# Optimization experiments

Measured on AMD Instinct MI355X. Metric: run time of the kernel, lower is better.

The kernel has to match this reference:

```python
import jax, jax.numpy as jnp
import numpy as np

EPS = 1e-7

def _attend(x):
    # x: [nc, w, h]; faithful to SelfAttention_1 with patch_size=3 (1x1 kernels, padding=1)
    nc, w, h = x.shape
    L = w * h
    # per-location 1x1 kernels, L2-normalized (kernels are [L, nc, 1, 1] in torch)
    k = x.reshape(nc, L).T + EPS                      # [L, nc]
    k = k / jnp.sqrt(jnp.sum(k * k, axis=1, keepdims=True))
    # conv2d with 1x1 kernels and padding=1 -> scores on padded grid [L, w+2, h+2]
    xp = jnp.pad(x, ((0, 0), (1, 1), (1, 1)))
    s = jnp.einsum('lc,cuv->luv', k, xp)              # [L, w+2, h+2]
    # avg_pool2d(3,1,pad=1) * 9 == 3x3 sum pooling with zero padding
    s = jax.lax.reduce_window(s, 0.0, jax.lax.add, (1, 3, 3), (1, 1, 1),
                              ((0, 0), (1, 1), (1, 1)))
    a = jax.nn.softmax(s, axis=0)                     # softmax over L (channel) axis
    # conv_transpose2d with 1x1 kernels, padding=1 == crop border then K^T @ A
    out = jnp.einsum('lc,luv->cuv', k, a[:, 1:-1, 1:-1])  # [nc, w, h]
    # torch: attention_scores.permute(0,2,3,1).view(w*h, -1) (raw reshape)
    att = jnp.transpose(a, (1, 2, 0)).reshape(L, -1)  # [L, (w+2)*(h+2)]
    return out, att


def setup_inputs() -> dict:
    key = jax.random.key(0)
    foreground = jax.random.normal(key, (4, 256, 64, 64), dtype=jnp.float32)
    return {"foreground": foreground}


def reference(foreground):
    out, att = jax.vmap(_attend)(foreground)          # out: [bz,nc,w,h], att: [bz,L,(w+2)*(h+2)]
    bz, L, M = att.shape
    return out, att.reshape(bz * L, M)
```

## Files before the change

kernel.cpp:

```cpp
#include <hip/hip_runtime.h>
#include <math.h>
#include <stdint.h>

#define LDIM 4096
#define NC   256
#define W66  66
#define P66  4356
#define BZ   4
#define EPSK 1e-7f

typedef _Float16 v8h __attribute__((ext_vector_type(8)));
typedef float v4f __attribute__((ext_vector_type(4)));

__device__ __forceinline__ void cp16(const void* g, void* l) {
    __builtin_amdgcn_global_load_lds(
        (const __attribute__((address_space(1))) void*)g,
        (__attribute__((address_space(3))) void*)l, 16, 0, 0);
}

__global__ __launch_bounds__(256) void rnorm_kernel(const float* __restrict__ x,
                                                    float* __restrict__ rnorm) {
    int idx = blockIdx.x * 256 + threadIdx.x;
    int b = idx >> 12;
    int l = idx & (LDIM - 1);
    const float* xb = x + (size_t)b * NC * LDIM + l;
    float s = 0.f;
#pragma unroll 8
    for (int c = 0; c < NC; ++c) {
        float v = xb[(size_t)c * LDIM] + EPSK;
        s += v * v;
    }
    rnorm[idx] = 1.0f / sqrtf(s);
}

__global__ __launch_bounds__(256) void kconv_kernel(const float* __restrict__ x,
                                                    const float* __restrict__ rn,
                                                    _Float16* __restrict__ Kcl,
                                                    _Float16* __restrict__ Klc) {
    __shared__ _Float16 t[64][72];
    int b = blockIdx.z, c0 = blockIdx.y * 64, l0 = blockIdx.x * 64;
    int tid = threadIdx.x;
    int r = tid >> 2, q = (tid & 3) * 16;
    const float* xr = x + ((size_t)(b * NC + c0 + r)) * LDIM + l0 + q;
    const float* rr = rn + b * LDIM + l0 + q;
    _Float16 h[16];
#pragma unroll
    for (int j = 0; j < 16; ++j)
        h[j] = (_Float16)((xr[j] + EPSK) * rr[j]);
    _Float16* kc = Kcl + ((size_t)(b * NC + c0 + r)) * LDIM + l0 + q;
    *(v8h*)kc = *(v8h*)h;
    *(v8h*)(kc + 8) = *(v8h*)(h + 8);
#pragma unroll
    for (int j = 0; j < 16; ++j) t[r][q + j] = h[j];
    __syncthreads();
    _Float16 g[16];
#pragma unroll
    for (int j = 0; j < 16; ++j) g[j] = t[q + j][r];
    _Float16* kl = Klc + ((size_t)(b * LDIM + l0 + r)) * NC + c0 + q;
    *(v8h*)kl = *(v8h*)g;
    *(v8h*)(kl + 8) = *(v8h*)(g + 8);
}

__global__ __launch_bounds__(256) void pool_kernel(const float* __restrict__ x,
                                                   float* __restrict__ Pm) {
    size_t idx = (size_t)blockIdx.x * 256 + threadIdx.x;
    int p = (int)(idx % P66);
    size_t bc = idx / P66;
    int u = p / W66, v = p % W66;
    const float* xbc = x + bc * (size_t)LDIM;
    int i0 = max(u - 2, 0), i1 = min(u, 63);
    int j0 = max(v - 2, 0), j1 = min(v, 63);
    float s = 0.f;
    for (int i = i0; i <= i1; ++i)
        for (int j = j0; j <= j1; ++j)
            s += xbc[i * 64 + j];
    Pm[idx] = s;
}

__global__ __launch_bounds__(256) void ptrans_kernel(const float* __restrict__ PoolF,
                                                     _Float16* __restrict__ Pm16) {
    __shared__ float t[64][65];
    int b = blockIdx.z, c0 = blockIdx.y * 64, p0 = blockIdx.x * 64;
    int tid = threadIdx.x;
    int r = tid >> 2, q = (tid & 3) * 16;
    const float* src = PoolF + ((size_t)(b * NC + c0 + r)) * P66 + p0 + q;
#pragma unroll
    for (int j = 0; j < 16; ++j) t[r][q + j] = src[j];
    __syncthreads();
    if (p0 + r < P66) {
        _Float16 g[16];
#pragma unroll
        for (int j = 0; j < 16; ++j) g[j] = (_Float16)t[q + j][r];
        _Float16* dst = Pm16 + ((size_t)(b * P66 + p0 + r)) * NC + c0 + q;
        *(v8h*)dst = *(v8h*)g;
        *(v8h*)(dst + 8) = *(v8h*)(g + 8);
    }
}

__global__ __launch_bounds__(256) void gemm1_mfma(const _Float16* __restrict__ Pm16,
                                                  const _Float16* __restrict__ Klc,
                                                  float* __restrict__ S) {
    __shared__ _Float16 As[128 * 32];
    __shared__ _Float16 Bs[128 * 32];
    int b = blockIdx.z;
    int p0 = blockIdx.y * 128;
    int l0 = blockIdx.x * 128;
    const _Float16* A = Pm16 + (size_t)b * P66 * NC;
    const _Float16* B = Klc + (size_t)b * LDIM * NC;
    float* C = S + (size_t)b * P66 * LDIM;
    int tid = threadIdx.x;
    int lane = tid & 63, wave = tid >> 6;
    int wm = (wave >> 1) * 64, wn = (wave & 1) * 64;
    int quad = lane >> 4, hn = lane & 15;
    int sr = tid >> 2, sk = (tid & 3) * 8;
    int pa0 = p0 + sr;      if (pa0 > P66 - 1) pa0 = P66 - 1;
    int pa1 = p0 + sr + 64; if (pa1 > P66 - 1) pa1 = P66 - 1;
    const _Float16* Ag0 = A + (size_t)pa0 * NC + sk;
    const _Float16* Ag1 = A + (size_t)pa1 * NC + sk;
    const _Float16* Bg0 = B + (size_t)(l0 + sr) * NC + sk;
    const _Float16* Bg1 = B + (size_t)(l0 + sr + 64) * NC + sk;
    char* lA = (char*)As + tid * 16;
    char* lB = (char*)Bs + tid * 16;
    v4f acc[4][4];
    v4f vz = {0.f, 0.f, 0.f, 0.f};
#pragma unroll
    for (int i = 0; i < 4; ++i)
#pragma unroll
        for (int j = 0; j < 4; ++j) acc[i][j] = vz;

    for (int k0 = 0; k0 < NC; k0 += 32) {
        __syncthreads();
        cp16(Ag0 + k0, lA);
        cp16(Ag1 + k0, lA + 4096);
        cp16(Bg0 + k0, lB);
        cp16(Bg1 + k0, lB + 4096);
        __syncthreads();
        v8h af[4], bfr[4];
#pragma unroll
        for (int t = 0; t < 4; ++t)
            af[t] = *(const v8h*)(As + (wm + t * 16 + hn) * 32 + quad * 8);
#pragma unroll
        for (int t = 0; t < 4; ++t)
            bfr[t] = *(const v8h*)(Bs + (wn + t * 16 + hn) * 32 + quad * 8);
#pragma unroll
        for (int i = 0; i < 4; ++i)
#pragma unroll
            for (int j = 0; j < 4; ++j)
                acc[i][j] = __builtin_amdgcn_mfma_f32_16x16x32_f16(af[i], bfr[j], acc[i][j], 0, 0, 0);
    }
#pragma unroll
    for (int i = 0; i < 4; ++i) {
        int pr = p0 + wm + i * 16 + quad * 4;
#pragma unroll
        for (int j = 0; j < 4; ++j) {
            int lc = l0 + wn + j * 16 + hn;
            float* Cp = C + (size_t)pr * LDIM + lc;
#pragma unroll
            for (int r = 0; r < 4; ++r)
                if (pr + r < P66) Cp[(size_t)r * LDIM] = acc[i][j][r];
        }
    }
}

__global__ __launch_bounds__(256) void softmax_kernel(float* __restrict__ att) {
    float* row = att + (size_t)blockIdx.x * LDIM;
    int tid = threadIdx.x;
    float4 v[4];
    float mx = -1e30f;
#pragma unroll
    for (int i = 0; i < 4; ++i) {
        v[i] = ((float4*)row)[tid + i * 256];
        mx = fmaxf(mx, fmaxf(fmaxf(v[i].x, v[i].y), fmaxf(v[i].z, v[i].w)));
    }
    __shared__ float sred[4];
    __shared__ float ssum[4];
#pragma unroll
    for (int off = 32; off > 0; off >>= 1) mx = fmaxf(mx, __shfl_xor(mx, off));
    if ((tid & 63) == 0) sred[tid >> 6] = mx;
    __syncthreads();
    float m4 = fmaxf(fmaxf(sred[0], sred[1]), fmaxf(sred[2], sred[3]));
    float sum = 0.f;
#pragma unroll
    for (int i = 0; i < 4; ++i) {
        v[i].x = __expf(v[i].x - m4);
        v[i].y = __expf(v[i].y - m4);
        v[i].z = __expf(v[i].z - m4);
        v[i].w = __expf(v[i].w - m4);
        sum += (v[i].x + v[i].y) + (v[i].z + v[i].w);
    }
#pragma unroll
    for (int off = 32; off > 0; off >>= 1) sum += __shfl_xor(sum, off);
    if ((tid & 63) == 0) ssum[tid >> 6] = sum;
    __syncthreads();
    float r = 1.0f / (ssum[0] + ssum[1] + ssum[2] + ssum[3]);
#pragma unroll
    for (int i = 0; i < 4; ++i) {
        v[i].x *= r; v[i].y *= r; v[i].z *= r; v[i].w *= r;
        ((float4*)row)[tid + i * 256] = v[i];
    }
}

__global__ __launch_bounds__(256) void gemm2_mfma(const _Float16* __restrict__ Kcl,
                                                  const float* __restrict__ attF,
                                                  float* __restrict__ outp) {
    __shared__ _Float16 As[128 * 32];
    __shared__ float BsF[32 * 32];
    int b = blockIdx.z;
    int c0 = blockIdx.x * 128;
    int i0 = blockIdx.y * 32;
    const _Float16* A = Kcl + (size_t)b * NC * LDIM;
    const float* Batt = attF + (size_t)b * P66 * LDIM;
    float* C = outp + (size_t)b * NC * LDIM;
    int tid = threadIdx.x;
    int lane = tid & 63, wave = tid >> 6;
    int wm = (wave >> 1) * 64, wn = (wave & 1) * 16;
    int quad = lane >> 4, hn = lane & 15;
    int sr = tid >> 2, sk = (tid & 3) * 8;
    const _Float16* Ag0 = A + (size_t)(c0 + sr) * LDIM + sk;
    const _Float16* Ag1 = A + (size_t)(c0 + sr + 64) * LDIM + sk;
    int br = tid >> 3;
    int bo = (((tid & 7) ^ (br & 7)) << 2);
    int ii = i0 + br;
    int p = ((ii >> 6) + 1) * W66 + (ii & 63) + 1;
    const float* Bg = Batt + (size_t)p * LDIM + bo;
    char* lA = (char*)As + tid * 16;
    char* lB = (char*)BsF + tid * 16;
    v4f acc[4];
    v4f vz = {0.f, 0.f, 0.f, 0.f};
#pragma unroll
    for (int i = 0; i < 4; ++i) acc[i] = vz;

    for (int k0 = 0; k0 < LDIM; k0 += 32) {
        __syncthreads();
        cp16(Ag0 + k0, lA);
        cp16(Ag1 + k0, lA + 4096);
        cp16(Bg + k0, lB);
        __syncthreads();
        v8h af[4];
#pragma unroll
        for (int t = 0; t < 4; ++t)
            af[t] = *(const v8h*)(As + (wm + t * 16 + hn) * 32 + quad * 8);
        int brow = wn + hn;
        int s0 = ((quad * 2 + 0) ^ (brow & 7)) << 2;
        int s1 = ((quad * 2 + 1) ^ (brow & 7)) << 2;
        v4f x0 = *(const v4f*)(BsF + brow * 32 + s0);
        v4f x1 = *(const v4f*)(BsF + brow * 32 + s1);
        v8h bfr;
#pragma unroll
        for (int j = 0; j < 4; ++j) { bfr[j] = (_Float16)x0[j]; bfr[j + 4] = (_Float16)x1[j]; }
#pragma unroll
        for (int i = 0; i < 4; ++i)
            acc[i] = __builtin_amdgcn_mfma_f32_16x16x32_f16(af[i], bfr, acc[i], 0, 0, 0);
    }
#pragma unroll
    for (int i = 0; i < 4; ++i) {
        int cr = c0 + wm + i * 16 + quad * 4;
        int ic = i0 + wn + hn;
        float* Cp = C + (size_t)cr * LDIM + ic;
#pragma unroll
        for (int r = 0; r < 4; ++r)
            Cp[(size_t)r * LDIM] = acc[i][r];
    }
}

extern "C" void kernel_launch(void* const* d_in, const int* in_sizes, int n_in,
                              void* d_out, int out_size, void* d_ws, size_t ws_size,
                              hipStream_t stream) {
    const float* x = (const float*)d_in[0];
    float* out = (float*)d_out;
    float* att = (float*)d_out + 4194304;
    float* rn = (float*)d_ws;
    _Float16* Kcl = (_Float16*)(rn + 16384);
    _Float16* Klc = Kcl + (size_t)BZ * NC * LDIM;
    float* PoolF = (float*)(Klc + (size_t)BZ * NC * LDIM);
    _Float16* Pm16 = (_Float16*)(PoolF + (size_t)BZ * NC * P66);

    rnorm_kernel<<<64, 256, 0, stream>>>(x, rn);
    kconv_kernel<<<dim3(64, 4, BZ), 256, 0, stream>>>(x, rn, Kcl, Klc);
    pool_kernel<<<17424, 256, 0, stream>>>(x, PoolF);
    ptrans_kernel<<<dim3(69, 4, BZ), 256, 0, stream>>>(PoolF, Pm16);
    gemm1_mfma<<<dim3(32, 35, BZ), 256, 0, stream>>>(Pm16, Klc, att);
    softmax_kernel<<<17424, 256, 0, stream>>>(att);
    gemm2_mfma<<<dim3(2, 128, BZ), 256, 0, stream>>>(Kcl, att, out);
}
```

Baseline: 658.0 us.

## Parallelize rnorm, use shared-memory separable pooling, vectorize loads, deepen gemm2 k-step

The rnorm kernel now splits the channel reduction across four waves per block and combines the partial sums in shared memory, so it launches four times as many blocks. The pool kernel stages each image in LDS and computes the 3x3 sum as a row pass followed by a column pass, replacing redundant global reads. kconv and ptrans switch from scalar to float4 global loads. gemm2 loads four 32-wide k-slices per synchronization, which cuts barrier count at the cost of about 48KB of LDS per block and possibly lower occupancy.

Measured after the change: 653.6 us. Within noise of the previous version (-0.7%).

```diff
diff --git a/kernel.cpp b/kernel.cpp
--- a/kernel.cpp
+++ b/kernel.cpp
@@ -20,17 +20,24 @@
 
 __global__ __launch_bounds__(256) void rnorm_kernel(const float* __restrict__ x,
                                                     float* __restrict__ rnorm) {
-    int idx = blockIdx.x * 256 + threadIdx.x;
-    int b = idx >> 12;
-    int l = idx & (LDIM - 1);
-    const float* xb = x + (size_t)b * NC * LDIM + l;
+    __shared__ float part[4][64];
+    int blk = blockIdx.x;
+    int b = blk >> 6;
+    int l0 = (blk & 63) << 6;
+    int lane = threadIdx.x & 63, cg = threadIdx.x >> 6;
+    const float* xb = x + (size_t)b * NC * LDIM + l0 + lane;
     float s = 0.f;
 #pragma unroll 8
-    for (int c = 0; c < NC; ++c) {
+    for (int c = cg * 64; c < cg * 64 + 64; ++c) {
         float v = xb[(size_t)c * LDIM] + EPSK;
         s += v * v;
     }
-    rnorm[idx] = 1.0f / sqrtf(s);
+    part[cg][lane] = s;
+    __syncthreads();
+    if (cg == 0) {
+        float t = part[0][lane] + part[1][lane] + part[2][lane] + part[3][lane];
+        rnorm[b * LDIM + l0 + lane] = 1.0f / sqrtf(t);
+    }
 }
 
 __global__ __launch_bounds__(256) void kconv_kernel(const float* __restrict__ x,
@@ -43,10 +50,18 @@
     int r = tid >> 2, q = (tid & 3) * 16;
     const float* xr = x + ((size_t)(b * NC + c0 + r)) * LDIM + l0 + q;
     const float* rr = rn + b * LDIM + l0 + q;
+    const float4* xr4 = (const float4*)xr;
+    const float4* rr4 = (const float4*)rr;
     _Float16 h[16];
 #pragma unroll
-    for (int j = 0; j < 16; ++j)
-        h[j] = (_Float16)((xr[j] + EPSK) * rr[j]);
+    for (int j4 = 0; j4 < 4; ++j4) {
+        float4 a = xr4[j4];
+        float4 w = rr4[j4];
+        h[j4 * 4 + 0] = (_Float16)((a.x + EPSK) * w.x);
+        h[j4 * 4 + 1] = (_Float16)((a.y + EPSK) * w.y);
+        h[j4 * 4 + 2] = (_Float16)((a.z + EPSK) * w.z);
+        h[j4 * 4 + 3] = (_Float16)((a.w + EPSK) * w.w);
+    }
     _Float16* kc = Kcl + ((size_t)(b * NC + c0 + r)) * LDIM + l0 + q;
     *(v8h*)kc = *(v8h*)h;
     *(v8h*)(kc + 8) = *(v8h*)(h + 8);
@@ -63,18 +78,41 @@
 
 __global__ __launch_bounds__(256) void pool_kernel(const float* __restrict__ x,
                                                    float* __restrict__ Pm) {
-    size_t idx = (size_t)blockIdx.x * 256 + threadIdx.x;
-    int p = (int)(idx % P66);
-    size_t bc = idx / P66;
-    int u = p / W66, v = p % W66;
-    const float* xbc = x + bc * (size_t)LDIM;
-    int i0 = max(u - 2, 0), i1 = min(u, 63);
-    int j0 = max(v - 2, 0), j1 = min(v, 63);
-    float s = 0.f;
-    for (int i = i0; i <= i1; ++i)
-        for (int j = j0; j <= j1; ++j)
-            s += xbc[i * 64 + j];
-    Pm[idx] = s;
+    __shared__ float img[64][68];
+    __shared__ float rs[64][68];
+    int bc = blockIdx.x;
+    const float* xbc = x + (size_t)bc * LDIM;
+    int tid = threadIdx.x;
+#pragma unroll
+    for (int it = 0; it < 4; ++it) {
+        int o = tid + it * 256;
+        float4 vv = ((const float4*)xbc)[o];
+        int u = o >> 4, j4 = (o & 15) << 2;
+        img[u][j4] = vv.x; img[u][j4 + 1] = vv.y; img[u][j4 + 2] = vv.z; img[u][j4 + 3] = vv.w;
+    }
+    __syncthreads();
+    {
+        int u = tid >> 2, g = tid & 3;
+        int v0 = g * 17, v1 = v0 + 17; if (v1 > 66) v1 = 66;
+        const float* row = img[u];
+        for (int v = v0; v < v1; ++v) {
+            int j0 = v - 2; if (j0 < 0) j0 = 0;
+            int j1 = v; if (j1 > 63) j1 = 63;
+            float s = 0.f;
+            for (int j = j0; j <= j1; ++j) s += row[j];
+            rs[u][v] = s;
+        }
+    }
+    __syncthreads();
+    float* Pout = Pm + (size_t)bc * P66;
+    for (int p = tid; p < P66; p += 256) {
+        int uu = p / W66, v = p - uu * W66;
+        int i0 = uu - 2; if (i0 < 0) i0 = 0;
+        int i1 = uu; if (i1 > 63) i1 = 63;
+        float s = 0.f;
+        for (int i = i0; i <= i1; ++i) s += rs[i][v];
+        Pout[p] = s;
+    }
 }
 
 __global__ __launch_bounds__(256) void ptrans_kernel(const float* __restrict__ PoolF,
@@ -84,8 +122,13 @@
     int tid = threadIdx.x;
     int r = tid >> 2, q = (tid & 3) * 16;
     const float* src = PoolF + ((size_t)(b * NC + c0 + r)) * P66 + p0 + q;
-#pragma unroll
-    for (int j = 0; j < 16; ++j) t[r][q + j] = src[j];
+    const float4* s4 = (const float4*)src;
+#pragma unroll
+    for (int j4 = 0; j4 < 4; ++j4) {
+        float4 a = s4[j4];
+        t[r][q + j4 * 4 + 0] = a.x; t[r][q + j4 * 4 + 1] = a.y;
+        t[r][q + j4 * 4 + 2] = a.z; t[r][q + j4 * 4 + 3] = a.w;
+    }
     __syncthreads();
     if (p0 + r < P66) {
         _Float16 g[16];
@@ -203,8 +246,8 @@
 __global__ __launch_bounds__(256) void gemm2_mfma(const _Float16* __restrict__ Kcl,
                                                   const float* __restrict__ attF,
                                                   float* __restrict__ outp) {
-    __shared__ _Float16 As[128 * 32];
-    __shared__ float BsF[32 * 32];
+    __shared__ _Float16 As[4][128 * 32];
+    __shared__ float BsF[4][32 * 32];
     int b = blockIdx.z;
     int c0 = blockIdx.x * 128;
     int i0 = blockIdx.y * 32;
@@ -216,8 +259,7 @@
     int wm = (wave >> 1) * 64, wn = (wave & 1) * 16;
     int quad = lane >> 4, hn = lane & 15;
     int sr = tid >> 2, sk = (tid & 3) * 8;
-    const _Float16* Ag0 = A + (size_t)(c0 + sr) * LDIM + sk;
-    const _Float16* Ag1 = A + (size_t)(c0 + sr + 64) * LDIM + sk;
+    const _Float16* Ag = A + (size_t)(c0 + sr) * LDIM + sk;
     int br = tid >> 3;
     int bo = (((tid & 7) ^ (br & 7)) << 2);
     int ii = i0 + br;
@@ -230,27 +272,35 @@
 #pragma unroll
     for (int i = 0; i < 4; ++i) acc[i] = vz;
 
-    for (int k0 = 0; k0 < LDIM; k0 += 32) {
+    for (int k0 = 0; k0 < LDIM; k0 += 128) {
         __syncthreads();
-        cp16(Ag0 + k0, lA);
-        cp16(Ag1 + k0, lA + 4096);
-        cp16(Bg + k0, lB);
+#pragma unroll
+        for (int j = 0; j < 4; ++j) {
+            cp16(Ag + k0 + j * 32, lA + j * 8192);
+            cp16(Ag + (size_t)64 * LDIM + k0 + j * 32, lA + j * 8192 + 4096);
+            cp16(Bg + k0 + j * 32, lB + j * 4096);
+        }
         __syncthreads();
-        v8h af[4];
-#pragma unroll
-        for (int t = 0; t < 4; ++t)
-            af[t] = *(const v8h*)(As + (wm + t * 16 + hn) * 32 + quad * 8);
-        int brow = wn + hn;
-        int s0 = ((quad * 2 + 0) ^ (brow & 7)) << 2;
-        int s1 = ((quad * 2 + 1) ^ (brow & 7)) << 2;
-        v4f x0 = *(const v4f*)(BsF + brow * 32 + s0);
-        v4f x1 = *(const v4f*)(BsF + brow * 32 + s1);
-        v8h bfr;
-#pragma unroll
-        for (int j = 0; j < 4; ++j) { bfr[j] = (_Float16)x0[j]; bfr[j + 4] = (_Float16)x1[j]; }
-#pragma unroll
-        for (int i = 0; i < 4; ++i)
-            acc[i] = __builtin_amdgcn_mfma_f32_16x16x32_f16(af[i], bfr, acc[i], 0, 0, 0);
+#pragma unroll
+        for (int j = 0; j < 4; ++j) {
+            const _Float16* Asl = (const _Float16*)As + j * 4096;
+            const float* Bsl = (const float*)BsF + j * 1024;
+            v8h af[4];
+#pragma unroll
+            for (int t = 0; t < 4; ++t)
+                af[t] = *(const v8h*)(Asl + (wm + t * 16 + hn) * 32 + quad * 8);
+            int brow = wn + hn;
+            int s0 = ((quad * 2 + 0) ^ (brow & 7)) << 2;
+            int s1 = ((quad * 2 + 1) ^ (brow & 7)) << 2;
+            v4f x0 = *(const v4f*)(Bsl + brow * 32 + s0);
+            v4f x1 = *(const v4f*)(Bsl + brow * 32 + s1);
+            v8h bfr;
+#pragma unroll
+            for (int jj = 0; jj < 4; ++jj) { bfr[jj] = (_Float16)x0[jj]; bfr[jj + 4] = (_Float16)x1[jj]; }
+#pragma unroll
+            for (int i = 0; i < 4; ++i)
+                acc[i] = __builtin_amdgcn_mfma_f32_16x16x32_f16(af[i], bfr, acc[i], 0, 0, 0);
+        }
     }
 #pragma unroll
     for (int i = 0; i < 4; ++i) {
@@ -275,9 +325,9 @@
     float* PoolF = (float*)(Klc + (size_t)BZ * NC * LDIM);
     _Float16* Pm16 = (_Float16*)(PoolF + (size_t)BZ * NC * P66);
 
-    rnorm_kernel<<<64, 256, 0, stream>>>(x, rn);
+    rnorm_kernel<<<256, 256, 0, stream>>>(x, rn);
     kconv_kernel<<<dim3(64, 4, BZ), 256, 0, stream>>>(x, rn, Kcl, Klc);
-    pool_kernel<<<17424, 256, 0, stream>>>(x, PoolF);
+    pool_kernel<<<BZ * NC, 256, 0, stream>>>(x, PoolF);
     ptrans_kernel<<<dim3(69, 4, BZ), 256, 0, stream>>>(PoolF, Pm16);
     gemm1_mfma<<<dim3(32, 35, BZ), 256, 0, stream>>>(Pm16, Klc, att);
     softmax_kernel<<<17424, 256, 0, stream>>>(att);
```
